# Kernel tuning notes

Measured on AMD Instinct MI355X. Metric: run time of the kernel, lower is better.

The kernel has to match this reference:

```python
import jax, jax.numpy as jnp
import numpy as np

N, F, H, C, E = 100000, 128, 128, 40, 1600000


def setup_inputs() -> dict:
    key = jax.random.key(0)
    ks = jax.random.split(key, 8)
    x = jax.random.normal(ks[0], (N, F), dtype=jnp.float32)
    edge_index = jax.random.randint(ks[1], (2, E), 0, N, dtype=jnp.int64)
    s = 0.05
    return {
        "x": x,
        "edge_index": edge_index,
        "eps1": jnp.float32(0.0),
        "w1": jax.random.normal(ks[2], (F, H), dtype=jnp.float32) * s,
        "b1": jnp.zeros((H,), jnp.float32),
        "w2": jax.random.normal(ks[3], (H, H), dtype=jnp.float32) * s,
        "b2": jnp.zeros((H,), jnp.float32),
        "eps2": jnp.float32(0.0),
        "w3": jax.random.normal(ks[4], (H, H), dtype=jnp.float32) * s,
        "b3": jnp.zeros((H,), jnp.float32),
        "w4": jax.random.normal(ks[5], (H, C), dtype=jnp.float32) * s,
        "b4": jnp.zeros((C,), jnp.float32),
    }


def _gin_aggregate(h, src, dst, eps, n):
    # sum_{j -> i} h_j  +  (1+eps) * h_i
    agg = jax.ops.segment_sum(h[src], dst, num_segments=n)
    return (1.0 + eps) * h + agg


def reference(x, edge_index, eps1, w1, b1, w2, b2, eps2, w3, b3, w4, b4):
    src, dst = edge_index[0], edge_index[1]
    n = x.shape[0]
    # conv1: GINConv with MLP = Lin-ReLU-Lin-ReLU
    h = _gin_aggregate(x, src, dst, eps1, n)
    h = jax.nn.relu(h @ w1 + b1)
    h = jax.nn.relu(h @ w2 + b2)
    h = jax.nn.relu(h)  # outer F.relu (idempotent, kept for faithfulness)
    # dropout: identity in eval mode
    # conv2: GINConv with MLP = Lin-ReLU-Lin
    h2 = _gin_aggregate(h, src, dst, eps2, n)
    h2 = jax.nn.relu(h2 @ w3 + b3)
    h2 = h2 @ w4 + b4
    return jax.nn.log_softmax(h2, axis=1)
```

## Files before the change

kernel.cpp:

```cpp
#include <hip/hip_runtime.h>
#include <hip/hip_fp16.h>
#include <math.h>

constexpr int F = 128;
constexpr int C = 40;
constexpr int LDH = 136;
constexpr int BSHIFT = 8;
constexpr int BSIZE = 1 << BSHIFT;
constexpr int CHUNK = 8192;

typedef __attribute__((ext_vector_type(8))) _Float16 half8;
typedef __attribute__((ext_vector_type(4))) float float4v;


__device__ void prep_conv(const float* in, __half* out, int n4, int blk) {
    int i = blk * 256 + threadIdx.x;
    if (i >= n4) return;
    float4 v = ((const float4*)in)[i];
    __half2 a = __floats2half2_rn(v.x, v.y);
    __half2 b = __floats2half2_rn(v.z, v.w);
    uint2 o;
    o.x = __builtin_bit_cast(unsigned, a);
    o.y = __builtin_bit_cast(unsigned, b);
    ((uint2*)out)[i] = o;
}

__device__ void prep_weight(const float* in, __half* outp, int Nin, int Npad) {
    __shared__ float lds[128 * 128];
    int t = threadIdx.x;
    int nf4 = 128 * Nin / 4;
    for (int i = t; i < nf4; i += 256)
        ((float4*)lds)[i] = ((const float4*)in)[i];
    __syncthreads();
    int total = Npad * 64;
    for (int i = t; i < total; i += 256) {
        int n = i >> 6, k2 = (i & 63) * 2;
        float lo = 0.f, hi = 0.f;
        if (n < Nin) {
            lo = lds[k2 * Nin + n];
            hi = lds[(k2 + 1) * Nin + n];
        }
        __half2 h = __floats2half2_rn(lo, hi);
        ((unsigned*)outp)[i] = __builtin_bit_cast(unsigned, h);
    }
}

__device__ void prep_hist(const int* dst, int E, int NB, int* coarse_count, int blk) {
    __shared__ int hist[512];
    int t = threadIdx.x;
    int c0 = blk * CHUNK;
    int cend = min(c0 + CHUNK, E);
    for (int i = t; i < NB; i += 256) hist[i] = 0;
    __syncthreads();
    for (int i = c0 + t; i < cend; i += 256)
        atomicAdd(&hist[dst[i] >> BSHIFT], 1);
    __syncthreads();
    for (int i = t; i < NB; i += 256)
        if (hist[i]) atomicAdd(&coarse_count[i], hist[i]);
}

__global__ __launch_bounds__(256) void prep_kernel(
        const float* __restrict__ x, __half* __restrict__ x_h, int n4, int Bconv,
        const float* __restrict__ w1, const float* __restrict__ w2,
        const float* __restrict__ w3, const float* __restrict__ w4,
        __half* __restrict__ w1t, __half* __restrict__ w2t,
        __half* __restrict__ w3t, __half* __restrict__ w4t,
        const int* __restrict__ dst, int E, int NB, int* __restrict__ coarse_count) {
    int b = blockIdx.x;
    if (b < Bconv) {
        prep_conv(x, x_h, n4, b);
    } else if (b < Bconv + 4) {
        switch (b - Bconv) {
            case 0: prep_weight(w1, w1t, 128, 128); break;
            case 1: prep_weight(w2, w2t, 128, 128); break;
            case 2: prep_weight(w3, w3t, 128, 128); break;
            default: prep_weight(w4, w4t, 40, 48); break;
        }
    } else {
        prep_hist(dst, E, NB, coarse_count, b - Bconv - 4);
    }
}


__global__ __launch_bounds__(512) void coarse_scan_kernel(const int* __restrict__ coarse_count,
                                                          int NB, int E,
                                                          int* __restrict__ coarse_start,
                                                          int* __restrict__ bucket_pos,
                                                          int* __restrict__ row_start, int N) {
    __shared__ int tmp[512];
    int t = threadIdx.x;
    int v = (t < NB) ? coarse_count[t] : 0;
    tmp[t] = v;
    __syncthreads();
    for (int d = 1; d < 512; d <<= 1) {
        int add = (t >= d) ? tmp[t - d] : 0;
        __syncthreads();
        tmp[t] += add;
        __syncthreads();
    }
    if (t < NB) {
        int ex = tmp[t] - v;
        coarse_start[t] = ex;
        bucket_pos[t] = ex;
    }
    if (t == 0) {
        coarse_start[NB] = E;
        row_start[N] = E;
    }
}

__global__ __launch_bounds__(256) void bucket_scatter_a_kernel(
        const int* __restrict__ src, const int* __restrict__ dst, int E, int NB,
        int* __restrict__ bucket_pos, unsigned* __restrict__ pairs) {
    __shared__ int hist[512];
    __shared__ int base[512];
    int t = threadIdx.x;
    int c0 = blockIdx.x * CHUNK;
    int cend = min(c0 + CHUNK, E);
    for (int i = t; i < NB; i += 256) hist[i] = 0;
    __syncthreads();
    for (int i = c0 + t; i < cend; i += 256)
        atomicAdd(&hist[dst[i] >> BSHIFT], 1);
    __syncthreads();
    for (int i = t; i < NB; i += 256) {
        int h = hist[i];
        base[i] = (h > 0) ? atomicAdd(&bucket_pos[i], h) : 0;
        hist[i] = 0;
    }
    __syncthreads();
    for (int i = c0 + t; i < cend; i += 256) {
        int d = dst[i];
        int b = d >> BSHIFT;
        int p = base[b] + atomicAdd(&hist[b], 1);
        pairs[p] = ((unsigned)(d & (BSIZE - 1)) << 24) | (unsigned)src[i];
    }
}

__global__ __launch_bounds__(256) void bucket_sort_kernel(const unsigned* __restrict__ pairs,
                                                          const int* __restrict__ coarse_start,
                                                          int N, int* __restrict__ row_start,
                                                          int* __restrict__ src_sorted) {
    __shared__ int hist[256];
    __shared__ int tmp[256];
    int b = blockIdx.x, t = threadIdx.x;
    int base = b << BSHIFT;
    int start = coarse_start[b];
    int end = coarse_start[b + 1];
    hist[t] = 0;
    __syncthreads();
    for (int i = start + t; i < end; i += 256)
        atomicAdd(&hist[pairs[i] >> 24], 1);
    __syncthreads();
    int v = hist[t];
    tmp[t] = v;
    __syncthreads();
    for (int d = 1; d < 256; d <<= 1) {
        int add = (t >= d) ? tmp[t - d] : 0;
        __syncthreads();
        tmp[t] += add;
        __syncthreads();
    }
    int ex = start + tmp[t] - v;
    if (base + t < N) row_start[base + t] = ex;
    hist[t] = ex;
    __syncthreads();
    for (int i = start + t; i < end; i += 256) {
        unsigned u = pairs[i];
        int p = atomicAdd(&hist[u >> 24], 1);
        src_sorted[p] = (int)(u & 0x00FFFFFFu);
    }
}


__global__ __launch_bounds__(256) void agg_f16_kernel(const __half* __restrict__ feat,
        const int* __restrict__ row_start, const int* __restrict__ src_sorted,
        const float* __restrict__ eps_ptr, __half* __restrict__ out, int N) {
    int wid = (int)((blockIdx.x * blockDim.x + threadIdx.x) >> 6);
    int lane = threadIdx.x & 63;
    if (wid >= N) return;
    int q = lane >> 4, l16 = lane & 15;
    int s = row_start[wid], e = row_start[wid + 1];
    __half2 A0, A1, A2, A3, B0, B1, B2, B3;
    __half2 C0, C1, C2, C3, D0, D1, D2, D3;
    A0 = A1 = A2 = A3 = B0 = B1 = B2 = B3 = __builtin_bit_cast(__half2, 0u);
    C0 = C1 = C2 = C3 = D0 = D1 = D2 = D3 = __builtin_bit_cast(__half2, 0u);
    int i = s + q;
    for (; i + 12 < e; i += 16) {
        int sv0 = src_sorted[i];
        int sv1 = src_sorted[i + 4];
        int sv2 = src_sorted[i + 8];
        int sv3 = src_sorted[i + 12];
        uint4 u0 = *(((const uint4*)(feat + (size_t)sv0 * F)) + l16);
        uint4 u1 = *(((const uint4*)(feat + (size_t)sv1 * F)) + l16);
        uint4 u2 = *(((const uint4*)(feat + (size_t)sv2 * F)) + l16);
        uint4 u3 = *(((const uint4*)(feat + (size_t)sv3 * F)) + l16);
        A0 = __hadd2(A0, __builtin_bit_cast(__half2, u0.x));
        A1 = __hadd2(A1, __builtin_bit_cast(__half2, u0.y));
        A2 = __hadd2(A2, __builtin_bit_cast(__half2, u0.z));
        A3 = __hadd2(A3, __builtin_bit_cast(__half2, u0.w));
        B0 = __hadd2(B0, __builtin_bit_cast(__half2, u1.x));
        B1 = __hadd2(B1, __builtin_bit_cast(__half2, u1.y));
        B2 = __hadd2(B2, __builtin_bit_cast(__half2, u1.z));
        B3 = __hadd2(B3, __builtin_bit_cast(__half2, u1.w));
        C0 = __hadd2(C0, __builtin_bit_cast(__half2, u2.x));
        C1 = __hadd2(C1, __builtin_bit_cast(__half2, u2.y));
        C2 = __hadd2(C2, __builtin_bit_cast(__half2, u2.z));
        C3 = __hadd2(C3, __builtin_bit_cast(__half2, u2.w));
        D0 = __hadd2(D0, __builtin_bit_cast(__half2, u3.x));
        D1 = __hadd2(D1, __builtin_bit_cast(__half2, u3.y));
        D2 = __hadd2(D2, __builtin_bit_cast(__half2, u3.z));
        D3 = __hadd2(D3, __builtin_bit_cast(__half2, u3.w));
    }
    for (; i + 4 < e; i += 8) {
        int sv0 = src_sorted[i];
        int sv1 = src_sorted[i + 4];
        uint4 u0 = *(((const uint4*)(feat + (size_t)sv0 * F)) + l16);
        uint4 u1 = *(((const uint4*)(feat + (size_t)sv1 * F)) + l16);
        A0 = __hadd2(A0, __builtin_bit_cast(__half2, u0.x));
        A1 = __hadd2(A1, __builtin_bit_cast(__half2, u0.y));
        A2 = __hadd2(A2, __builtin_bit_cast(__half2, u0.z));
        A3 = __hadd2(A3, __builtin_bit_cast(__half2, u0.w));
        B0 = __hadd2(B0, __builtin_bit_cast(__half2, u1.x));
        B1 = __hadd2(B1, __builtin_bit_cast(__half2, u1.y));
        B2 = __hadd2(B2, __builtin_bit_cast(__half2, u1.z));
        B3 = __hadd2(B3, __builtin_bit_cast(__half2, u1.w));
    }
    if (i < e) {
        int sv = src_sorted[i];
        uint4 u = *(((const uint4*)(feat + (size_t)sv * F)) + l16);
        A0 = __hadd2(A0, __builtin_bit_cast(__half2, u.x));
        A1 = __hadd2(A1, __builtin_bit_cast(__half2, u.y));
        A2 = __hadd2(A2, __builtin_bit_cast(__half2, u.z));
        A3 = __hadd2(A3, __builtin_bit_cast(__half2, u.w));
    }
    float a[8];
    {
        float2 fa, fb, fc, fd;
        fa = __half22float2(A0); fb = __half22float2(B0);
        fc = __half22float2(C0); fd = __half22float2(D0);
        a[0] = (fa.x + fb.x) + (fc.x + fd.x); a[1] = (fa.y + fb.y) + (fc.y + fd.y);
        fa = __half22float2(A1); fb = __half22float2(B1);
        fc = __half22float2(C1); fd = __half22float2(D1);
        a[2] = (fa.x + fb.x) + (fc.x + fd.x); a[3] = (fa.y + fb.y) + (fc.y + fd.y);
        fa = __half22float2(A2); fb = __half22float2(B2);
        fc = __half22float2(C2); fd = __half22float2(D2);
        a[4] = (fa.x + fb.x) + (fc.x + fd.x); a[5] = (fa.y + fb.y) + (fc.y + fd.y);
        fa = __half22float2(A3); fb = __half22float2(B3);
        fc = __half22float2(C3); fd = __half22float2(D3);
        a[6] = (fa.x + fb.x) + (fc.x + fd.x); a[7] = (fa.y + fb.y) + (fc.y + fd.y);
    }
#pragma unroll
    for (int j = 0; j < 8; ++j) {
        a[j] += __shfl_xor(a[j], 16);
        a[j] += __shfl_xor(a[j], 32);
    }
    if (q == 0) {
        float ep1 = 1.0f + *eps_ptr;
        uint4 u = *(((const uint4*)(feat + (size_t)wid * F)) + l16);
        float2 s0 = __half22float2(__builtin_bit_cast(__half2, u.x));
        float2 s1 = __half22float2(__builtin_bit_cast(__half2, u.y));
        float2 s2 = __half22float2(__builtin_bit_cast(__half2, u.z));
        float2 s3 = __half22float2(__builtin_bit_cast(__half2, u.w));
        a[0] = fmaf(ep1, s0.x, a[0]); a[1] = fmaf(ep1, s0.y, a[1]);
        a[2] = fmaf(ep1, s1.x, a[2]); a[3] = fmaf(ep1, s1.y, a[3]);
        a[4] = fmaf(ep1, s2.x, a[4]); a[5] = fmaf(ep1, s2.y, a[5]);
        a[6] = fmaf(ep1, s3.x, a[6]); a[7] = fmaf(ep1, s3.y, a[7]);
        uint4 ou;
        ou.x = __builtin_bit_cast(unsigned, __floats2half2_rn(a[0], a[1]));
        ou.y = __builtin_bit_cast(unsigned, __floats2half2_rn(a[2], a[3]));
        ou.z = __builtin_bit_cast(unsigned, __floats2half2_rn(a[4], a[5]));
        ou.w = __builtin_bit_cast(unsigned, __floats2half2_rn(a[6], a[7]));
        *(((uint4*)(out + (size_t)wid * F)) + l16) = ou;
    }
}


__global__ __launch_bounds__(256) void mlp1_mfma_kernel(const __half* __restrict__ A,
        const __half* __restrict__ w1t, const float* __restrict__ b1,
        const __half* __restrict__ w2t, const float* __restrict__ b2,
        __half* __restrict__ out, int N) {
    __shared__ __half ldsA[64 * LDH];
    __shared__ __half ldsW[128 * LDH];
    __shared__ float ldsB[256];
    int t = threadIdx.x;
    int wave = t >> 6, lane = t & 63, quad = lane >> 4, l16 = lane & 15;
    int br = blockIdx.x * 64;
    if (t < 128) ldsB[t] = b1[t];
    else         ldsB[t] = b2[t - 128];
    for (int i = t; i < 1024; i += 256) {
        int r = i >> 4, c = i & 15;
        int gr = br + r;
        uint4 v = make_uint4(0u, 0u, 0u, 0u);
        if (gr < N) v = *((const uint4*)(A + (size_t)gr * F + c * 8));
        *((uint4*)&ldsA[r * LDH + c * 8]) = v;
    }
    for (int i = t; i < 2048; i += 256) {
        int r = i >> 4, c = i & 15;
        *((uint4*)&ldsW[r * LDH + c * 8]) = *((const uint4*)(w1t + r * 128 + c * 8));
    }
    __syncthreads();

    int ct0 = wave * 2;
    float4v acc[4][2];
    float4v zero = {0.f, 0.f, 0.f, 0.f};
#pragma unroll
    for (int i = 0; i < 4; ++i)
#pragma unroll
        for (int j = 0; j < 2; ++j) acc[i][j] = zero;

#pragma unroll
    for (int ks = 0; ks < 4; ++ks) {
        half8 af[4], wf[2];
#pragma unroll
        for (int i = 0; i < 4; ++i)
            af[i] = *((const half8*)&ldsA[(i * 16 + l16) * LDH + ks * 32 + quad * 8]);
#pragma unroll
        for (int j = 0; j < 2; ++j)
            wf[j] = *((const half8*)&ldsW[((ct0 + j) * 16 + l16) * LDH + ks * 32 + quad * 8]);
#pragma unroll
        for (int i = 0; i < 4; ++i)
#pragma unroll
            for (int j = 0; j < 2; ++j)
                acc[i][j] = __builtin_amdgcn_mfma_f32_16x16x32_f16(wf[j], af[i], acc[i][j], 0, 0, 0);
    }
    __syncthreads();
#pragma unroll
    for (int j = 0; j < 2; ++j) {
        int c = ct0 + j;
        float4 bb = *((const float4*)&ldsB[c * 16 + quad * 4]);
#pragma unroll
        for (int i = 0; i < 4; ++i) {
            float v0 = acc[i][j][0] + bb.x; v0 = v0 > 0.f ? v0 : 0.f;
            float v1 = acc[i][j][1] + bb.y; v1 = v1 > 0.f ? v1 : 0.f;
            float v2 = acc[i][j][2] + bb.z; v2 = v2 > 0.f ? v2 : 0.f;
            float v3 = acc[i][j][3] + bb.w; v3 = v3 > 0.f ? v3 : 0.f;
            __half2 h0 = __floats2half2_rn(v0, v1);
            __half2 h1 = __floats2half2_rn(v2, v3);
            uint2 o;
            o.x = __builtin_bit_cast(unsigned, h0);
            o.y = __builtin_bit_cast(unsigned, h1);
            *((uint2*)&ldsA[(i * 16 + l16) * LDH + c * 16 + quad * 4]) = o;
        }
    }
    for (int i = t; i < 2048; i += 256) {
        int r = i >> 4, c = i & 15;
        *((uint4*)&ldsW[r * LDH + c * 8]) = *((const uint4*)(w2t + r * 128 + c * 8));
    }
    __syncthreads();

#pragma unroll
    for (int i = 0; i < 4; ++i)
#pragma unroll
        for (int j = 0; j < 2; ++j) acc[i][j] = zero;
#pragma unroll
    for (int ks = 0; ks < 4; ++ks) {
        half8 af[4], wf[2];
#pragma unroll
        for (int i = 0; i < 4; ++i)
            af[i] = *((const half8*)&ldsA[(i * 16 + l16) * LDH + ks * 32 + quad * 8]);
#pragma unroll
        for (int j = 0; j < 2; ++j)
            wf[j] = *((const half8*)&ldsW[((ct0 + j) * 16 + l16) * LDH + ks * 32 + quad * 8]);
#pragma unroll
        for (int i = 0; i < 4; ++i)
#pragma unroll
            for (int j = 0; j < 2; ++j)
                acc[i][j] = __builtin_amdgcn_mfma_f32_16x16x32_f16(wf[j], af[i], acc[i][j], 0, 0, 0);
    }
    __syncthreads();
#pragma unroll
    for (int j = 0; j < 2; ++j) {
        int c = ct0 + j;
        float4 bb = *((const float4*)&ldsB[128 + c * 16 + quad * 4]);
#pragma unroll
        for (int i = 0; i < 4; ++i) {
            float v0 = acc[i][j][0] + bb.x; v0 = v0 > 0.f ? v0 : 0.f;
            float v1 = acc[i][j][1] + bb.y; v1 = v1 > 0.f ? v1 : 0.f;
            float v2 = acc[i][j][2] + bb.z; v2 = v2 > 0.f ? v2 : 0.f;
            float v3 = acc[i][j][3] + bb.w; v3 = v3 > 0.f ? v3 : 0.f;
            __half2 h0 = __floats2half2_rn(v0, v1);
            __half2 h1 = __floats2half2_rn(v2, v3);
            uint2 o;
            o.x = __builtin_bit_cast(unsigned, h0);
            o.y = __builtin_bit_cast(unsigned, h1);
            *((uint2*)&ldsA[(i * 16 + l16) * LDH + c * 16 + quad * 4]) = o;
        }
    }
    __syncthreads();
    for (int i = t; i < 1024; i += 256) {
        int r = i >> 4, c = i & 15;
        int gr = br + r;
        if (gr < N)
            *((uint4*)(out + (size_t)gr * F + c * 8)) = *((const uint4*)&ldsA[r * LDH + c * 8]);
    }
}


__global__ __launch_bounds__(256) void mlp2_mfma_kernel(const __half* __restrict__ A,
        const __half* __restrict__ w3t, const float* __restrict__ b3,
        const __half* __restrict__ w4t, const float* __restrict__ b4,
        float* __restrict__ out, int N) {
    __shared__ __half ldsA[64 * LDH];
    __shared__ __half ldsW[128 * LDH];
    __shared__ float ldsB[176];
    int t = threadIdx.x;
    int wave = t >> 6, lane = t & 63, quad = lane >> 4, l16 = lane & 15;
    int br = blockIdx.x * 64;
    if (t < 128) ldsB[t] = b3[t];
    else if (t < 176) ldsB[t] = (t - 128 < C) ? b4[t - 128] : 0.f;
    for (int i = t; i < 1024; i += 256) {
        int r = i >> 4, c = i & 15;
        int gr = br + r;
        uint4 v = make_uint4(0u, 0u, 0u, 0u);
        if (gr < N) v = *((const uint4*)(A + (size_t)gr * F + c * 8));
        *((uint4*)&ldsA[r * LDH + c * 8]) = v;
    }
    for (int i = t; i < 2048; i += 256) {
        int r = i >> 4, c = i & 15;
        *((uint4*)&ldsW[r * LDH + c * 8]) = *((const uint4*)(w3t + r * 128 + c * 8));
    }
    __syncthreads();

    int ct0 = wave * 2;
    float4v acc[4][2];
    float4v zero = {0.f, 0.f, 0.f, 0.f};
#pragma unroll
    for (int i = 0; i < 4; ++i)
#pragma unroll
        for (int j = 0; j < 2; ++j) acc[i][j] = zero;
#pragma unroll
    for (int ks = 0; ks < 4; ++ks) {
        half8 af[4], wf[2];
#pragma unroll
        for (int i = 0; i < 4; ++i)
            af[i] = *((const half8*)&ldsA[(i * 16 + l16) * LDH + ks * 32 + quad * 8]);
#pragma unroll
        for (int j = 0; j < 2; ++j)
            wf[j] = *((const half8*)&ldsW[((ct0 + j) * 16 + l16) * LDH + ks * 32 + quad * 8]);
#pragma unroll
        for (int i = 0; i < 4; ++i)
#pragma unroll
            for (int j = 0; j < 2; ++j)
                acc[i][j] = __builtin_amdgcn_mfma_f32_16x16x32_f16(wf[j], af[i], acc[i][j], 0, 0, 0);
    }
    __syncthreads();
#pragma unroll
    for (int j = 0; j < 2; ++j) {
        int c = ct0 + j;
        float4 bb = *((const float4*)&ldsB[c * 16 + quad * 4]);
#pragma unroll
        for (int i = 0; i < 4; ++i) {
            float v0 = acc[i][j][0] + bb.x; v0 = v0 > 0.f ? v0 : 0.f;
            float v1 = acc[i][j][1] + bb.y; v1 = v1 > 0.f ? v1 : 0.f;
            float v2 = acc[i][j][2] + bb.z; v2 = v2 > 0.f ? v2 : 0.f;
            float v3 = acc[i][j][3] + bb.w; v3 = v3 > 0.f ? v3 : 0.f;
            __half2 h0 = __floats2half2_rn(v0, v1);
            __half2 h1 = __floats2half2_rn(v2, v3);
            uint2 o;
            o.x = __builtin_bit_cast(unsigned, h0);
            o.y = __builtin_bit_cast(unsigned, h1);
            *((uint2*)&ldsA[(i * 16 + l16) * LDH + c * 16 + quad * 4]) = o;
        }
    }
    for (int i = t; i < 768; i += 256) {
        int r = i >> 4, c = i & 15;
        *((uint4*)&ldsW[r * LDH + c * 8]) = *((const uint4*)(w4t + r * 128 + c * 8));
    }
    __syncthreads();

    float4v acc4[3];
#pragma unroll
    for (int c = 0; c < 3; ++c) acc4[c] = zero;
#pragma unroll
    for (int ks = 0; ks < 4; ++ks) {
        half8 af = *((const half8*)&ldsA[(wave * 16 + l16) * LDH + ks * 32 + quad * 8]);
#pragma unroll
        for (int c = 0; c < 3; ++c) {
            half8 wf = *((const half8*)&ldsW[(c * 16 + l16) * LDH + ks * 32 + quad * 8]);
            acc4[c] = __builtin_amdgcn_mfma_f32_16x16x32_f16(wf, af, acc4[c], 0, 0, 0);
        }
    }
    float lv[3][4];
#pragma unroll
    for (int c = 0; c < 3; ++c) {
        float4 bb = *((const float4*)&ldsB[128 + c * 16 + quad * 4]);
        lv[c][0] = acc4[c][0] + bb.x;
        lv[c][1] = acc4[c][1] + bb.y;
        lv[c][2] = acc4[c][2] + bb.z;
        lv[c][3] = acc4[c][3] + bb.w;
    }
    bool tile2ok = (quad < 2);
    float m = -1e30f;
#pragma unroll
    for (int c = 0; c < 3; ++c) {
        if (c == 2 && !tile2ok) continue;
#pragma unroll
        for (int r = 0; r < 4; ++r) m = fmaxf(m, lv[c][r]);
    }
    m = fmaxf(m, __shfl_xor(m, 16));
    m = fmaxf(m, __shfl_xor(m, 32));
    float ssum = 0.f;
#pragma unroll
    for (int c = 0; c < 3; ++c) {
        if (c == 2 && !tile2ok) continue;
#pragma unroll
        for (int r = 0; r < 4; ++r) ssum += __expf(lv[c][r] - m);
    }
    ssum += __shfl_xor(ssum, 16);
    ssum += __shfl_xor(ssum, 32);
    float L = m + __logf(ssum);
    int node = br + wave * 16 + l16;
    if (node < N) {
#pragma unroll
        for (int c = 0; c < 3; ++c) {
            if (c == 2 && !tile2ok) continue;
            float4 o = make_float4(lv[c][0] - L, lv[c][1] - L, lv[c][2] - L, lv[c][3] - L);
            *((float4*)(out + (size_t)node * C + c * 16 + quad * 4)) = o;
        }
    }
}


extern "C" void kernel_launch(void* const* d_in, const int* in_sizes, int n_in,
                              void* d_out, int out_size, void* d_ws, size_t ws_size,
                              hipStream_t stream) {
    const float* x    = (const float*)d_in[0];
    const int*   ei   = (const int*)d_in[1];
    const float* eps1 = (const float*)d_in[2];
    const float* w1   = (const float*)d_in[3];
    const float* b1   = (const float*)d_in[4];
    const float* w2   = (const float*)d_in[5];
    const float* b2   = (const float*)d_in[6];
    const float* eps2 = (const float*)d_in[7];
    const float* w3   = (const float*)d_in[8];
    const float* b3   = (const float*)d_in[9];
    const float* w4   = (const float*)d_in[10];
    const float* b4   = (const float*)d_in[11];
    float* out = (float*)d_out;

    int N = in_sizes[0] / F;
    int E = in_sizes[1] / 2;
    const int* src = ei;
    const int* dst = ei + E;

    int NB = (N + BSIZE - 1) >> BSHIFT;
    int BA = (E + CHUNK - 1) / CHUNK;
    int n4 = N * F / 4;
    int Bconv = (n4 + 255) / 256;

    __half* x_h  = (__half*)d_ws;
    __half* h0_h = x_h + (size_t)N * F;
    __half* h_h  = h0_h + (size_t)N * F;
    __half* w1t  = h_h + (size_t)N * F;
    __half* w2t  = w1t + 128 * 128;
    __half* w3t  = w2t + 128 * 128;
    __half* w4t  = w3t + 128 * 128;
    unsigned* pairs   = (unsigned*)(w4t + 48 * 128);
    int* row_start    = (int*)(pairs + E);
    int* src_sorted   = row_start + (N + 1);
    int* coarse_count = src_sorted + E;
    int* coarse_start = coarse_count + 512;
    int* bucket_pos   = coarse_start + 513;

    hipMemsetAsync(coarse_count, 0, (size_t)NB * sizeof(int), stream);
    prep_kernel<<<Bconv + 4 + BA, 256, 0, stream>>>(x, x_h, n4, Bconv,
                                                    w1, w2, w3, w4, w1t, w2t, w3t, w4t,
                                                    dst, E, NB, coarse_count);

    coarse_scan_kernel<<<1, 512, 0, stream>>>(coarse_count, NB, E, coarse_start, bucket_pos,
                                              row_start, N);
    bucket_scatter_a_kernel<<<BA, 256, 0, stream>>>(src, dst, E, NB, bucket_pos, pairs);
    bucket_sort_kernel<<<NB, 256, 0, stream>>>(pairs, coarse_start, N, row_start, src_sorted);

    agg_f16_kernel<<<(N + 3) / 4, 256, 0, stream>>>(x_h, row_start, src_sorted, eps1, h0_h, N);
    mlp1_mfma_kernel<<<(N + 63) / 64, 256, 0, stream>>>(h0_h, w1t, b1, w2t, b2, h_h, N);
    agg_f16_kernel<<<(N + 3) / 4, 256, 0, stream>>>(h_h, row_start, src_sorted, eps2, h0_h, N);
    mlp2_mfma_kernel<<<(N + 63) / 64, 256, 0, stream>>>(h0_h, w3t, b3, w4t, b4, out, N);
}
```

Baseline: 358.4 us.

## Fuse GIN neighbor aggregation into MLP kernels via LDS staging

```diff
diff --git a/kernel.cpp b/kernel.cpp
--- a/kernel.cpp
+++ b/kernel.cpp
@@ -7,7 +7,7 @@
 constexpr int LDH = 136;
 constexpr int BSHIFT = 8;
 constexpr int BSIZE = 1 << BSHIFT;
-constexpr int CHUNK = 8192;
+constexpr int CHUNK = 4096;
 
 typedef __attribute__((ext_vector_type(8))) _Float16 half8;
 typedef __attribute__((ext_vector_type(4))) float float4v;
@@ -172,19 +172,22 @@
 }
 
 
-__global__ __launch_bounds__(256) void agg_f16_kernel(const __half* __restrict__ feat,
+__device__ __forceinline__ void agg_node(const __half* __restrict__ feat,
         const int* __restrict__ row_start, const int* __restrict__ src_sorted,
-        const float* __restrict__ eps_ptr, __half* __restrict__ out, int N) {
-    int wid = (int)((blockIdx.x * blockDim.x + threadIdx.x) >> 6);
-    int lane = threadIdx.x & 63;
-    if (wid >= N) return;
-    int q = lane >> 4, l16 = lane & 15;
+        float ep1, __half* __restrict__ ldsA, int ln, int wid, int N, int quad, int l16) {
+    if (wid >= N) {
+        if (quad == 0) {
+            uint4 z = make_uint4(0u, 0u, 0u, 0u);
+            *((uint4*)&ldsA[ln * LDH + l16 * 8]) = z;
+        }
+        return;
+    }
     int s = row_start[wid], e = row_start[wid + 1];
     __half2 A0, A1, A2, A3, B0, B1, B2, B3;
     __half2 C0, C1, C2, C3, D0, D1, D2, D3;
     A0 = A1 = A2 = A3 = B0 = B1 = B2 = B3 = __builtin_bit_cast(__half2, 0u);
     C0 = C1 = C2 = C3 = D0 = D1 = D2 = D3 = __builtin_bit_cast(__half2, 0u);
-    int i = s + q;
+    int i = s + quad;
     for (; i + 12 < e; i += 16) {
         int sv0 = src_sorted[i];
         int sv1 = src_sorted[i + 4];
@@ -254,8 +257,7 @@
         a[j] += __shfl_xor(a[j], 16);
         a[j] += __shfl_xor(a[j], 32);
     }
-    if (q == 0) {
-        float ep1 = 1.0f + *eps_ptr;
+    if (quad == 0) {
         uint4 u = *(((const uint4*)(feat + (size_t)wid * F)) + l16);
         float2 s0 = __half22float2(__builtin_bit_cast(__half2, u.x));
         float2 s1 = __half22float2(__builtin_bit_cast(__half2, u.y));
@@ -270,12 +272,14 @@
         ou.y = __builtin_bit_cast(unsigned, __floats2half2_rn(a[2], a[3]));
         ou.z = __builtin_bit_cast(unsigned, __floats2half2_rn(a[4], a[5]));
         ou.w = __builtin_bit_cast(unsigned, __floats2half2_rn(a[6], a[7]));
-        *(((uint4*)(out + (size_t)wid * F)) + l16) = ou;
-    }
-}
-
-
-__global__ __launch_bounds__(256) void mlp1_mfma_kernel(const __half* __restrict__ A,
+        *((uint4*)&ldsA[ln * LDH + l16 * 8]) = ou;
+    }
+}
+
+
+__global__ __launch_bounds__(256) void gin1_kernel(const __half* __restrict__ feat,
+        const int* __restrict__ row_start, const int* __restrict__ src_sorted,
+        const float* __restrict__ eps_ptr,
         const __half* __restrict__ w1t, const float* __restrict__ b1,
         const __half* __restrict__ w2t, const float* __restrict__ b2,
         __half* __restrict__ out, int N) {
@@ -287,12 +291,11 @@
     int br = blockIdx.x * 64;
     if (t < 128) ldsB[t] = b1[t];
     else         ldsB[t] = b2[t - 128];
-    for (int i = t; i < 1024; i += 256) {
-        int r = i >> 4, c = i & 15;
-        int gr = br + r;
-        uint4 v = make_uint4(0u, 0u, 0u, 0u);
-        if (gr < N) v = *((const uint4*)(A + (size_t)gr * F + c * 8));
-        *((uint4*)&ldsA[r * LDH + c * 8]) = v;
+    float ep1 = 1.0f + *eps_ptr;
+#pragma unroll 1
+    for (int j = 0; j < 16; ++j) {
+        int ln = wave * 16 + j;
+        agg_node(feat, row_start, src_sorted, ep1, ldsA, ln, br + ln, N, quad, l16);
     }
     for (int i = t; i < 2048; i += 256) {
         int r = i >> 4, c = i & 15;
@@ -396,7 +399,9 @@
 }
 
 
-__global__ __launch_bounds__(256) void mlp2_mfma_kernel(const __half* __restrict__ A,
+__global__ __launch_bounds__(256) void gin2_kernel(const __half* __restrict__ feat,
+        const int* __restrict__ row_start, const int* __restrict__ src_sorted,
+        const float* __restrict__ eps_ptr,
         const __half* __restrict__ w3t, const float* __restrict__ b3,
         const __half* __restrict__ w4t, const float* __restrict__ b4,
         float* __restrict__ out, int N) {
@@ -408,12 +413,11 @@
     int br = blockIdx.x * 64;
     if (t < 128) ldsB[t] = b3[t];
     else if (t < 176) ldsB[t] = (t - 128 < C) ? b4[t - 128] : 0.f;
-    for (int i = t; i < 1024; i += 256) {
-        int r = i >> 4, c = i & 15;
-        int gr = br + r;
-        uint4 v = make_uint4(0u, 0u, 0u, 0u);
-        if (gr < N) v = *((const uint4*)(A + (size_t)gr * F + c * 8));
-        *((uint4*)&ldsA[r * LDH + c * 8]) = v;
+    float ep1 = 1.0f + *eps_ptr;
+#pragma unroll 1
+    for (int j = 0; j < 16; ++j) {
+        int ln = wave * 16 + j;
+        agg_node(feat, row_start, src_sorted, ep1, ldsA, ln, br + ln, N, quad, l16);
     }
     for (int i = t; i < 2048; i += 256) {
         int r = i >> 4, c = i & 15;
@@ -549,8 +553,7 @@
     int Bconv = (n4 + 255) / 256;
 
     __half* x_h  = (__half*)d_ws;
-    __half* h0_h = x_h + (size_t)N * F;
-    __half* h_h  = h0_h + (size_t)N * F;
+    __half* h_h  = x_h + (size_t)N * F;
     __half* w1t  = h_h + (size_t)N * F;
     __half* w2t  = w1t + 128 * 128;
     __half* w3t  = w2t + 128 * 128;
@@ -572,8 +575,8 @@
     bucket_scatter_a_kernel<<<BA, 256, 0, stream>>>(src, dst, E, NB, bucket_pos, pairs);
     bucket_sort_kernel<<<NB, 256, 0, stream>>>(pairs, coarse_start, N, row_start, src_sorted);
 
-    agg_f16_kernel<<<(N + 3) / 4, 256, 0, stream>>>(x_h, row_start, src_sorted, eps1, h0_h, N);
-    mlp1_mfma_kernel<<<(N + 63) / 64, 256, 0, stream>>>(h0_h, w1t, b1, w2t, b2, h_h, N);
-    agg_f16_kernel<<<(N + 3) / 4, 256, 0, stream>>>(h_h, row_start, src_sorted, eps2, h0_h, N);
-    mlp2_mfma_kernel<<<(N + 63) / 64, 256, 0, stream>>>(h0_h, w3t, b3, w4t, b4, out, N);
-}
+    gin1_kernel<<<(N + 63) / 64, 256, 0, stream>>>(x_h, row_start, src_sorted, eps1,
+                                                   w1t, b1, w2t, b2, h_h, N);
+    gin2_kernel<<<(N + 63) / 64, 256, 0, stream>>>(h_h, row_start, src_sorted, eps2,
+                                                   w3t, b3, w4t, b4, out, N);
+}
```

Result: slower. 465.9 us (+30.0%).
